# Kernel optimization log

Hardware: AMD Instinct MI355X
Metric: run time of the kernel (lower is better)

## Reference

```python
import jax, jax.numpy as jnp
import numpy as np

N_LAYER = 4
N_HEAD = 1
D = 64        # feature dim d (Z has d+1 columns)
N = 512       # context length (Z has N+1 rows)
B = 512
VAR = 1e-4
RUN_MODE = 1  # run_mode==1 -> residual with gamma; run_mode==0 -> R = attention_sum


def setup_inputs() -> dict:
    key = jax.random.key(0)
    k1, k2 = jax.random.split(key)
    Z = jax.random.normal(k1, (B, N + 1, D + 1), dtype=jnp.float32)
    allparam = jax.random.normal(k2, (N_LAYER, N_HEAD, 2, D, D), dtype=jnp.float32) * VAR
    gamma = jnp.zeros((N_LAYER,), jnp.float32)  # requires_grad only if run_mode==1 (torch)
    alpha = jnp.ones((N_LAYER,), jnp.float32)
    return {"Z": Z, "allparam": allparam, "gamma": gamma, "alpha": alpha}


def _project(allparam):
    # Mirrors zero_p() and identity_q() (done in torch under no_grad, in-place):
    #   P <- 0 ; Q <- mean(diag(Q)) * I
    d = allparam.shape[-1]
    P = jnp.zeros_like(allparam[:, :, 0])                                # [L,H,d,d]
    Q = allparam[:, :, 1]
    diag_mean = jnp.mean(jnp.diagonal(Q, axis1=-2, axis2=-1), axis=-1)   # [L,H]
    Qp = diag_mean[..., None, None] * jnp.eye(d, dtype=allparam.dtype)
    return jnp.stack([P, Qp], axis=2)                                    # [L,H,2,d,d]


def _pad_full(M, corner):
    # M: [H,d,d] -> [H,d+1,d+1] zero-padded, with [d,d] = corner
    H, d, _ = M.shape
    Mf = jnp.zeros((H, d + 1, d + 1), M.dtype).at[:, :d, :d].set(M)
    return Mf.at[:, d, d].set(corner)


def _layer_attention(Z, P, Q):
    # Z: [B,N+1,d+1]; P,Q: [H,d,d]. Non-softmax linear attention.
    n = Z.shape[1] - 1
    Pf = _pad_full(P, 1.0)  # P_full with P_full[d,d] = 1
    Qf = _pad_full(Q, 0.0)
    # Attn[b,h,n,m] = Z[b,n,:] Qf[h] Z[b,m,:]
    Attn = jnp.einsum('bni,hij,bmj->bhnm', Z, Qf, Z)
    key = jnp.einsum('hij,bnj->bhni', Pf, Z)
    # A = eye(N+1) with A[N,N]=0  ==> drop last key row (column N of Attn)
    out = jnp.einsum('bhnm,bhmi->bni', Attn[:, :, :, :n], key[:, :, :n, :])
    return out / n  # heads summed inside the einsum


def reference(Z, allparam, gamma, alpha):
    params = _project(allparam)  # [L,H,2,d,d]
    R = jnp.zeros_like(Z)
    for i in range(params.shape[0]):  # loop over n_layer (small, fixed)
        attn_sum = _layer_attention(Z, params[i, :, 0], params[i, :, 1])
        if RUN_MODE == 0:
            R = attn_sum
        else:
            R = R * gamma[i] + attn_sum
        Z = Z + R * alpha[i]
    return Z
```

## Files before the change

### kernel.cpp

```cpp
#include <hip/hip_runtime.h>

#define NROW 513
#define NCOL 65
#define DD   64
#define NN   512
#define NLAYER 4
#define TPB  1024
#define NGRP 16


__launch_bounds__(TPB)
__global__ void tf_kernel(const float* __restrict__ Zin,
                          const float* __restrict__ allparam,
                          const float* __restrict__ gam,
                          const float* __restrict__ alp,
                          float* __restrict__ out) {
    __shared__ float Zs[NROW * NCOL];
    __shared__ float rS[NROW];
    __shared__ float sred[NGRP][DD];
    __shared__ float sv[DD];
    __shared__ float qs[NLAYER];

    const int tid = threadIdx.x;
    const int b = blockIdx.x;
    const long base = (long)b * (NROW * NCOL);

    if (tid < 64) {
        for (int l = 0; l < NLAYER; ++l) {
            float v = allparam[l * 8192 + 4096 + tid * 65];
            #pragma unroll
            for (int off = 32; off > 0; off >>= 1)
                v += __shfl_down(v, off, 64);
            if (tid == 0) qs[l] = v * (1.0f / 64.0f);
        }
    }

    for (int idx = tid; idx < NROW * NCOL; idx += TPB) {
        float v = Zin[base + idx];
        Zs[idx] = v;
        if (idx % NCOL != DD) out[base + idx] = v;
    }
    for (int n = tid; n < NROW; n += TPB) rS[n] = 0.0f;
    __syncthreads();

    for (int l = 0; l < NLAYER; ++l) {
        {
            const int j = tid & 63;
            const int g = tid >> 6;
            const int m0 = g * (NN / NGRP);
            float p = 0.0f;
            #pragma unroll 4
            for (int m = m0; m < m0 + NN / NGRP; ++m)
                p += Zs[m * NCOL + DD] * Zs[m * NCOL + j];
            sred[g][j] = p;
        }
        __syncthreads();
        if (tid < 64) {
            float p = 0.0f;
            #pragma unroll
            for (int g = 0; g < NGRP; ++g) p += sred[g][tid];
            sv[tid] = p;
        }
        __syncthreads();

        const float c  = qs[l] * (1.0f / (float)NN);
        const float gm = gam[l];
        const float al = alp[l];
        for (int n = tid; n < NROW; n += TPB) {
            float dot = 0.0f;
            #pragma unroll
            for (int j = 0; j < DD; ++j) dot += Zs[n * NCOL + j] * sv[j];
            const float rr = rS[n] * gm + c * dot;
            rS[n] = rr;
            Zs[n * NCOL + DD] += rr * al;
        }
        __syncthreads();
    }

    for (int n = tid; n < NROW; n += TPB)
        out[base + n * NCOL + DD] = Zs[n * NCOL + DD];
}

extern "C" void kernel_launch(void* const* d_in, const int* in_sizes, int n_in,
                              void* d_out, int out_size, void* d_ws, size_t ws_size,
                              hipStream_t stream) {
    const float* Z        = (const float*)d_in[0];
    const float* allparam = (const float*)d_in[1];
    const float* gam      = (const float*)d_in[2];
    const float* alp      = (const float*)d_in[3];
    float* out = (float*)d_out;
    tf_kernel<<<dim3(512), dim3(TPB), 0, stream>>>(Z, allparam, gam, alp, out);
}
```

Measured before the change: 151.5 us.

## Reformulate layers via Gram matrix on MFMA and stream Z without shared staging

Since only the last column of Z changes across layers, the kernel precomputes the 64x64 Gram matrix X^T X with bf16 MFMA, plus the vector X^T y. It then runs the four-layer recurrence on a 64-vector u in a single wave, and applies the result as one final matrix-vector product per row. The full Z tile is no longer staged in shared memory, which cuts LDS footprint so several blocks can share a CU, and the output is written with float4 copies. The trade-off is bf16 rounding in the Gram matrix, which may perturb accuracy, plus extra global reads of Z.

```diff
diff --git a/kernel.cpp b/kernel.cpp
--- a/kernel.cpp
+++ b/kernel.cpp
@@ -5,80 +5,157 @@
 #define DD   64
 #define NN   512
 #define NLAYER 4
-#define TPB  1024
-#define NGRP 16
+#define TPB  512
+#define NWAVE 8
 
+typedef float f32x16 __attribute__((ext_vector_type(16)));
+typedef short s16x8  __attribute__((ext_vector_type(8)));
 
-__launch_bounds__(TPB)
+__device__ __forceinline__ short bf16_rne(float f) {
+    unsigned u = __builtin_bit_cast(unsigned, f);
+    u += 0x7FFFu + ((u >> 16) & 1u);
+    return (short)(u >> 16);
+}
+
+__launch_bounds__(TPB, 4)
 __global__ void tf_kernel(const float* __restrict__ Zin,
                           const float* __restrict__ allparam,
                           const float* __restrict__ gam,
                           const float* __restrict__ alp,
                           float* __restrict__ out) {
-    __shared__ float Zs[NROW * NCOL];
-    __shared__ float rS[NROW];
-    __shared__ float sred[NGRP][DD];
-    __shared__ float sv[DD];
-    __shared__ float qs[NLAYER];
+    __shared__ float yl[NN];
+    __shared__ float Gl[DD][DD + 1];
+    __shared__ float s1l[DD];
+    __shared__ float ul[DD];
+    __shared__ float xul[NROW];
+    __shared__ float qsl[NLAYER];
 
-    const int tid = threadIdx.x;
-    const int b = blockIdx.x;
-    const long base = (long)b * (NROW * NCOL);
+    const int tid  = threadIdx.x;
+    const int w    = tid >> 6;
+    const int lane = tid & 63;
+    const int half = lane >> 5;
+    const int lc   = lane & 31;
+    const long base = (long)blockIdx.x * (NROW * NCOL);
 
+    for (int i = tid; i < DD * (DD + 1); i += TPB) ((float*)Gl)[i] = 0.0f;
+    if (tid < DD) { s1l[tid] = 0.0f; ul[tid] = 0.0f; }
+    if (tid < NN) yl[tid] = Zin[base + (long)tid * NCOL + DD];
     if (tid < 64) {
         for (int l = 0; l < NLAYER; ++l) {
             float v = allparam[l * 8192 + 4096 + tid * 65];
             #pragma unroll
-            for (int off = 32; off > 0; off >>= 1)
-                v += __shfl_down(v, off, 64);
-            if (tid == 0) qs[l] = v * (1.0f / 64.0f);
+            for (int off = 32; off > 0; off >>= 1) v += __shfl_down(v, off, 64);
+            if (tid == 0) qsl[l] = v * (1.0f / 64.0f);
         }
     }
-
-    for (int idx = tid; idx < NROW * NCOL; idx += TPB) {
-        float v = Zin[base + idx];
-        Zs[idx] = v;
-        if (idx % NCOL != DD) out[base + idx] = v;
-    }
-    for (int n = tid; n < NROW; n += TPB) rS[n] = 0.0f;
     __syncthreads();
 
-    for (int l = 0; l < NLAYER; ++l) {
-        {
-            const int j = tid & 63;
-            const int g = tid >> 6;
-            const int m0 = g * (NN / NGRP);
-            float p = 0.0f;
-            #pragma unroll 4
-            for (int m = m0; m < m0 + NN / NGRP; ++m)
-                p += Zs[m * NCOL + DD] * Zs[m * NCOL + j];
-            sred[g][j] = p;
+    {
+        f32x16 acc00, acc01, acc10, acc11;
+        #pragma unroll
+        for (int r = 0; r < 16; ++r) { acc00[r] = 0.f; acc01[r] = 0.f; acc10[r] = 0.f; acc11[r] = 0.f; }
+        float sp0 = 0.f, sp1 = 0.f;
+
+        #pragma unroll
+        for (int sl = 0; sl < 4; ++sl) {
+            const int rbase = w * 64 + sl * 16 + half * 8;
+            s16x8 f0, f1;
+            const float* rp = Zin + base + (long)rbase * NCOL + lc;
+            #pragma unroll
+            for (int e = 0; e < 8; ++e) {
+                float a0 = rp[0];
+                float a1 = rp[32];
+                float yv = yl[rbase + e];
+                sp0 += yv * a0;
+                sp1 += yv * a1;
+                f0[e] = bf16_rne(a0);
+                f1[e] = bf16_rne(a1);
+                rp += NCOL;
+            }
+            acc00 = __builtin_amdgcn_mfma_f32_32x32x16_bf16(f0, f0, acc00, 0, 0, 0);
+            acc01 = __builtin_amdgcn_mfma_f32_32x32x16_bf16(f0, f1, acc01, 0, 0, 0);
+            acc10 = __builtin_amdgcn_mfma_f32_32x32x16_bf16(f1, f0, acc10, 0, 0, 0);
+            acc11 = __builtin_amdgcn_mfma_f32_32x32x16_bf16(f1, f1, acc11, 0, 0, 0);
         }
-        __syncthreads();
-        if (tid < 64) {
-            float p = 0.0f;
+
+        sp0 += __shfl_xor(sp0, 32, 64);
+        sp1 += __shfl_xor(sp1, 32, 64);
+        if (half == 0) {
+            atomicAdd(&s1l[lc], sp0);
+            atomicAdd(&s1l[32 + lc], sp1);
+        }
+        #pragma unroll
+        for (int r = 0; r < 16; ++r) {
+            const int row = (r & 3) + 8 * (r >> 2) + 4 * half;
+            atomicAdd(&Gl[row][lc],           acc00[r]);
+            atomicAdd(&Gl[row][32 + lc],      acc01[r]);
+            atomicAdd(&Gl[32 + row][lc],      acc10[r]);
+            atomicAdd(&Gl[32 + row][32 + lc], acc11[r]);
+        }
+    }
+    __syncthreads();
+
+    if (tid < 64) {
+        const int j = tid;
+        const float s1j = s1l[j];
+        float u = 0.f, rho = 0.f;
+        for (int l = 0; l < NLAYER; ++l) {
+            float dot = 0.f;
+            #pragma unroll 8
+            for (int k = 0; k < DD; ++k) dot += Gl[j][k] * ul[k];
+            const float s = s1j + dot;
+            rho = gam[l] * rho + (qsl[l] * (1.0f / (float)NN)) * s;
+            u += alp[l] * rho;
+            ul[j] = u;
+        }
+    }
+    __syncthreads();
+
+    {
+        const float ucol = ul[lane];
+        for (int n = w; n < NROW; n += NWAVE) {
+            float p = Zin[base + (long)n * NCOL + lane] * ucol;
             #pragma unroll
-            for (int g = 0; g < NGRP; ++g) p += sred[g][tid];
-            sv[tid] = p;
+            for (int off = 32; off > 0; off >>= 1) p += __shfl_xor(p, off, 64);
+            if (lane == 0) xul[n] = p;
         }
-        __syncthreads();
+    }
+    __syncthreads();
 
-        const float c  = qs[l] * (1.0f / (float)NN);
-        const float gm = gam[l];
-        const float al = alp[l];
-        for (int n = tid; n < NROW; n += TPB) {
-            float dot = 0.0f;
-            #pragma unroll
-            for (int j = 0; j < DD; ++j) dot += Zs[n * NCOL + j] * sv[j];
-            const float rr = rS[n] * gm + c * dot;
-            rS[n] = rr;
-            Zs[n * NCOL + DD] += rr * al;
+    {
+        const long gbeg = base;
+        const long gend = base + (long)NROW * NCOL;
+        const long abeg = (gbeg + 3) & ~3L;
+        const long aend = gend & ~3L;
+        const int hcnt = (int)(abeg - gbeg);
+        if (tid < hcnt) {
+            const long g = gbeg + tid;
+            const int li = (int)(g - base);
+            float v = Zin[g];
+            if (li % NCOL == DD) v += xul[li / NCOL];
+            out[g] = v;
         }
-        __syncthreads();
+        const int tcnt = (int)(gend - aend);
+        if (tid >= 64 && tid < 64 + tcnt) {
+            const long g = aend + (tid - 64);
+            const int li = (int)(g - base);
+            float v = Zin[g];
+            if (li % NCOL == DD) v += xul[li / NCOL];
+            out[g] = v;
+        }
+        for (long a = abeg + (long)tid * 4; a < aend; a += (long)TPB * 4) {
+            float4 v = *(const float4*)(Zin + a);
+            const int li = (int)(a - base);
+            const int j = li % NCOL;
+            if (j >= NCOL - 4) {
+                if (j == DD)          v.x += xul[li / NCOL];
+                else if (j == DD - 1) v.y += xul[(li + 1) / NCOL];
+                else if (j == DD - 2) v.z += xul[(li + 2) / NCOL];
+                else                  v.w += xul[(li + 3) / NCOL];
+            }
+            *(float4*)(out + a) = v;
+        }
     }
-
-    for (int n = tid; n < NROW; n += TPB)
-        out[base + n * NCOL + DD] = Zs[n * NCOL + DD];
 }
 
 extern "C" void kernel_launch(void* const* d_in, const int* in_sizes, int n_in,
@@ -88,6 +165,6 @@
     const float* allparam = (const float*)d_in[1];
     const float* gam      = (const float*)d_in[2];
     const float* alp      = (const float*)d_in[3];
-    float* out = (float*)d_out;
-    tf_kernel<<<dim3(512), dim3(TPB), 0, stream>>>(Z, allparam, gam, alp, out);
+    float* outp = (float*)d_out;
+    tf_kernel<<<dim3(512), dim3(TPB), 0, stream>>>(Z, allparam, gam, alp, outp);
 }
```

After: 241.4 us. +59.3%, slower.
